# Kernel optimization log

Hardware: AMD Instinct MI355X
Metric: run time of the kernel (lower is better)

## Reference

```python
import jax, jax.numpy as jnp
import numpy as np

NUM_NODES = 100_000
NUM_EDGES = 3_200_000
THETA = 1.0  # module hyperparameter (default 1.0)


def setup_inputs() -> dict:
    key = jax.random.key(0)
    k_v, k_src, k_dst, k_t1, k_t2, k_r = jax.random.split(key, 6)
    v = jax.random.normal(k_v, (NUM_NODES,), dtype=jnp.float32)
    src = jax.random.randint(k_src, (NUM_EDGES,), 0, NUM_NODES, dtype=jnp.int32)
    dst = jax.random.randint(k_dst, (NUM_EDGES,), 0, NUM_NODES, dtype=jnp.int32)
    theta_sd_1 = jax.random.normal(k_t1, (NUM_EDGES,), dtype=jnp.float32) * 0.1
    theta_sd_2 = jax.random.normal(k_t2, (NUM_EDGES,), dtype=jnp.float32) * 0.1
    # conductance = 1/resistance, resistance in (0.5, 2.0) -> conductance in (0.5, 2.0)
    conductance = 1.0 / jax.random.uniform(k_r, (NUM_EDGES,), dtype=jnp.float32, minval=0.5, maxval=2.0)
    return {"t": 0, "v": v, "src": src, "dst": dst,
            "theta_sd_1": theta_sd_1, "theta_sd_2": theta_sd_2,
            "conductance": conductance}


def reference(t, v, src, dst, theta_sd_1, theta_sd_2, conductance):
    # per-edge gated current: g(vs, vd) = relu(theta1*(vs - vd) + theta2)
    diff = v[src] - v[dst]                                   # [E]
    current = conductance * jax.nn.relu(theta_sd_1 * diff + theta_sd_2)  # [E]
    incoming = jax.ops.segment_sum(current, dst, num_segments=NUM_NODES)  # [N]
    outgoing = jax.ops.segment_sum(current, src, num_segments=NUM_NODES)  # [N]
    return (incoming - outgoing) / THETA
```

## Files before the change

kernel.cpp:

```cpp
#include <hip/hip_runtime.h>
#include <hip/hip_fp16.h>


#define RANGE_LOG 15
#define RANGE     (1 << RANGE_LOG)
#define NBIN      4
#define P0_BLK    256
#define P0_EPT    4
#define P0_EPB    (P0_BLK * P0_EPT)
#define CAP       (2 * P0_EPB)
#define P1_BLK    1024
#define NSLICE    32

__global__ __launch_bounds__(P0_BLK) void p0_bin_kernel(
    const float* __restrict__ v,
    const int*   __restrict__ src,
    const int*   __restrict__ dst,
    const float* __restrict__ t1,
    const float* __restrict__ t2,
    const float* __restrict__ cond,
    unsigned*    __restrict__ bins,
    int*         __restrict__ cnt,
    int E, int G)
{
    __shared__ unsigned sbuf[NBIN][CAP];
    __shared__ int scnt[NBIN];

    if (threadIdx.x < NBIN) scnt[threadIdx.x] = 0;
    __syncthreads();

    const int blk = blockIdx.x;
    const int i0  = blk * P0_EPB + (int)threadIdx.x * P0_EPT;

    #define EMIT(node, mag, signbit)                                        \
        {                                                                   \
            int rr = (node) >> RANGE_LOG;                                   \
            unsigned lo = (unsigned)((node) & (RANGE - 1));                 \
            unsigned hb = (unsigned)__half_as_ushort(__float2half(mag));    \
            unsigned en = (lo << 17) | ((unsigned)(signbit) << 16) | hb;    \
            int idx = atomicAdd(&scnt[rr], 1);                              \
            sbuf[rr][idx] = en;                                             \
        }

    if (i0 + P0_EPT <= E) {
        int4   s4 = *(const int4*)  (src  + i0);
        int4   d4 = *(const int4*)  (dst  + i0);
        float4 a4 = *(const float4*)(t1   + i0);
        float4 b4 = *(const float4*)(t2   + i0);
        float4 c4 = *(const float4*)(cond + i0);

        float vs0 = v[s4.x], vs1 = v[s4.y], vs2 = v[s4.z], vs3 = v[s4.w];
        float vd0 = v[d4.x], vd1 = v[d4.y], vd2 = v[d4.z], vd3 = v[d4.w];

        float x0 = fmaf(a4.x, vs0 - vd0, b4.x);
        float x1 = fmaf(a4.y, vs1 - vd1, b4.y);
        float x2 = fmaf(a4.z, vs2 - vd2, b4.z);
        float x3 = fmaf(a4.w, vs3 - vd3, b4.w);

        if (x0 > 0.0f) { float c = c4.x * x0; EMIT(d4.x, c, 0u) EMIT(s4.x, c, 1u) }
        if (x1 > 0.0f) { float c = c4.y * x1; EMIT(d4.y, c, 0u) EMIT(s4.y, c, 1u) }
        if (x2 > 0.0f) { float c = c4.z * x2; EMIT(d4.z, c, 0u) EMIT(s4.z, c, 1u) }
        if (x3 > 0.0f) { float c = c4.w * x3; EMIT(d4.w, c, 0u) EMIT(s4.w, c, 1u) }
    } else {
        for (int i = i0; i < E; ++i) {
            int s = src[i], d = dst[i];
            float x = fmaf(t1[i], v[s] - v[d], t2[i]);
            if (x > 0.0f) { float c = cond[i] * x; EMIT(d, c, 0u) EMIT(s, c, 1u) }
        }
    }
    #undef EMIT

    __syncthreads();
    for (int r = 0; r < NBIN; ++r) {
        int c = scnt[r];
        unsigned* g = bins + ((size_t)r * G + blk) * CAP;
        for (int j = threadIdx.x; j < c; j += P0_BLK) g[j] = sbuf[r][j];
    }
    if (threadIdx.x < NBIN) cnt[threadIdx.x * G + blk] = scnt[threadIdx.x];
}

__global__ __launch_bounds__(P1_BLK) void p1_accum_kernel(
    const unsigned* __restrict__ bins,
    const int*      __restrict__ cnt,
    float*          __restrict__ partial,
    int N, int G)
{
    __shared__ __align__(16) float acc[RANGE];

    const int r    = blockIdx.x / NSLICE;
    const int s    = blockIdx.x % NSLICE;
    const int base = r << RANGE_LOG;
    const int len  = min(RANGE, N - base);

    for (int i = threadIdx.x; i < RANGE; i += P1_BLK) acc[i] = 0.0f;
    __syncthreads();

    const int segPer = (G + NSLICE - 1) / NSLICE;
    const int g0 = s * segPer;
    const int g1 = min(G, g0 + segPer);

    for (int g = g0; g < g1; ++g) {
        const int c = cnt[r * G + g];
        const unsigned* p = bins + ((size_t)r * G + g) * CAP;
        for (int j = threadIdx.x; j < c; j += P1_BLK) {
            unsigned e = p[j];
            int   lo  = (int)(e >> 17);
            float mag = __half2float(__ushort_as_half((unsigned short)(e & 0xFFFFu)));
            atomicAdd(&acc[lo], (e & 0x10000u) ? -mag : mag);
        }
    }

    __syncthreads();
    float* op = partial + (size_t)s * N + base;
    const int len4 = len & ~3;
    for (int i = (int)threadIdx.x * 4; i < len4; i += P1_BLK * 4)
        *(float4*)(op + i) = *(const float4*)&acc[i];
    for (int i = len4 + (int)threadIdx.x; i < len; i += P1_BLK)
        op[i] = acc[i];
}

__global__ __launch_bounds__(256) void reduce_kernel(
    const float* __restrict__ partial, float* __restrict__ out, int N4)
{
    int n = blockIdx.x * blockDim.x + threadIdx.x;
    if (n < N4) {
        float4 sm = make_float4(0.f, 0.f, 0.f, 0.f);
        for (int p = 0; p < NSLICE; ++p) {
            float4 q = ((const float4*)partial)[(size_t)p * N4 + n];
            sm.x += q.x; sm.y += q.y; sm.z += q.z; sm.w += q.w;
        }
        ((float4*)out)[n] = sm;
    }
}

__global__ __launch_bounds__(256) void reduce_scalar_kernel(
    const float* __restrict__ partial, float* __restrict__ out, int N)
{
    int n = blockIdx.x * blockDim.x + threadIdx.x;
    if (n < N) {
        float sm = 0.0f;
        for (int p = 0; p < NSLICE; ++p) sm += partial[(size_t)p * N + n];
        out[n] = sm;
    }
}

__global__ __launch_bounds__(256) void atomic_fallback_kernel(
    const float* __restrict__ v, const int* __restrict__ src, const int* __restrict__ dst,
    const float* __restrict__ t1, const float* __restrict__ t2, const float* __restrict__ cond,
    float* __restrict__ out, int E)
{
    int i = blockIdx.x * blockDim.x + threadIdx.x;
    int stride = gridDim.x * blockDim.x;
    for (; i < E; i += stride) {
        int s = src[i], d = dst[i];
        float x = fmaf(t1[i], v[s] - v[d], t2[i]);
        if (x > 0.0f) {
            float c = cond[i] * x;
            atomicAdd(&out[d], c);
            atomicAdd(&out[s], -c);
        }
    }
}

extern "C" void kernel_launch(void* const* d_in, const int* in_sizes, int n_in,
                              void* d_out, int out_size, void* d_ws, size_t ws_size,
                              hipStream_t stream) {
    const float* v    = (const float*)d_in[1];
    const int*   src  = (const int*)  d_in[2];
    const int*   dst  = (const int*)  d_in[3];
    const float* t1   = (const float*)d_in[4];
    const float* t2   = (const float*)d_in[5];
    const float* cond = (const float*)d_in[6];
    float* out = (float*)d_out;
    const int E = in_sizes[2];
    const int N = out_size;

    const int G = (E + P0_EPB - 1) / P0_EPB;

    const size_t binBytes = ((size_t)NBIN * G * CAP * 4 + 255) & ~(size_t)255;
    const size_t cntBytes = ((size_t)NBIN * G * 4 + 255) & ~(size_t)255;
    const size_t parBytes = (size_t)NSLICE * N * sizeof(float);

    const bool ok = (N <= NBIN * RANGE) &&
                    (binBytes + cntBytes + parBytes <= ws_size);

    if (ok) {
        unsigned* bins    = (unsigned*)d_ws;
        int*      cnt     = (int*)((char*)d_ws + binBytes);
        float*    partial = (float*)((char*)d_ws + binBytes + cntBytes);

        p0_bin_kernel<<<G, P0_BLK, 0, stream>>>(v, src, dst, t1, t2, cond,
                                                bins, cnt, E, G);

        const int R = (N + RANGE - 1) / RANGE;
        p1_accum_kernel<<<R * NSLICE, P1_BLK, 0, stream>>>(bins, cnt, partial, N, G);

        if ((N & 3) == 0) {
            int n4 = N / 4;
            reduce_kernel<<<(n4 + 255) / 256, 256, 0, stream>>>(partial, out, n4);
        } else {
            reduce_scalar_kernel<<<(N + 255) / 256, 256, 0, stream>>>(partial, out, N);
        }
    } else {
        hipMemsetAsync(out, 0, (size_t)N * sizeof(float), stream);
        int grid = (E + 255) / 256;
        if (grid > 2048) grid = 2048;
        atomic_fallback_kernel<<<grid, 256, 0, stream>>>(v, src, dst, t1, t2, cond, out, E);
    }
}
```

Before: 89.27 us.

## Compact binned edge entries into per-range global buffers via atomic cursors

The binning pass used to write each block's entries into fixed-capacity per-block slots. It now reserves space in one contiguous buffer per node range through a global atomic cursor and writes the entries there compactly. The accumulation pass then splits each range's contiguous entry list evenly across slices, instead of looping over per-block segments with separate counts. The node range is halved and the bin count doubled, which shrinks the shared accumulator per block. In exchange it adds a memset launch and global atomics, and it silently drops entries if a block overflows the 512-entry shared staging capacity or the estimated global capacity.

Result: faster. 87.24 us (-2.3%).

```diff
diff --git a/kernel.cpp b/kernel.cpp
--- a/kernel.cpp
+++ b/kernel.cpp
@@ -2,44 +2,43 @@
 #include <hip/hip_fp16.h>
 
 
-#define RANGE_LOG 15
-#define RANGE     (1 << RANGE_LOG)
-#define NBIN      4
-#define P0_BLK    256
-#define P0_EPT    4
-#define P0_EPB    (P0_BLK * P0_EPT)
-#define CAP       (2 * P0_EPB)
-#define P1_BLK    1024
-#define NSLICE    32
-
-__global__ __launch_bounds__(P0_BLK) void p0_bin_kernel(
+#define RL      14
+#define RANGE   (1 << RL)
+#define NB      8
+#define P0_BLK  256
+#define P0_EPT  4
+#define P0_EPB  (P0_BLK * P0_EPT)
+#define SCAP    512
+#define P1_BLK  1024
+#define NSLICE  32
+
+__global__ __launch_bounds__(P0_BLK) void p0_kernel(
     const float* __restrict__ v,
     const int*   __restrict__ src,
     const int*   __restrict__ dst,
     const float* __restrict__ t1,
     const float* __restrict__ t2,
     const float* __restrict__ cond,
-    unsigned*    __restrict__ bins,
-    int*         __restrict__ cnt,
-    int E, int G)
-{
-    __shared__ unsigned sbuf[NBIN][CAP];
-    __shared__ int scnt[NBIN];
-
-    if (threadIdx.x < NBIN) scnt[threadIdx.x] = 0;
-    __syncthreads();
-
-    const int blk = blockIdx.x;
-    const int i0  = blk * P0_EPB + (int)threadIdx.x * P0_EPT;
-
-    #define EMIT(node, mag, signbit)                                        \
-        {                                                                   \
-            int rr = (node) >> RANGE_LOG;                                   \
-            unsigned lo = (unsigned)((node) & (RANGE - 1));                 \
-            unsigned hb = (unsigned)__half_as_ushort(__float2half(mag));    \
-            unsigned en = (lo << 17) | ((unsigned)(signbit) << 16) | hb;    \
-            int idx = atomicAdd(&scnt[rr], 1);                              \
-            sbuf[rr][idx] = en;                                             \
+    unsigned*    __restrict__ entries,
+    int*         __restrict__ cursors,
+    int E, int EC)
+{
+    __shared__ unsigned sbuf[NB][SCAP];
+    __shared__ int scnt[NB], gbase[NB];
+
+    if (threadIdx.x < NB) scnt[threadIdx.x] = 0;
+    __syncthreads();
+
+    const int i0 = blockIdx.x * P0_EPB + (int)threadIdx.x * P0_EPT;
+
+    #define EMIT(node, mag, signbit)                                         \
+        {                                                                    \
+            int rr = (node) >> RL;                                           \
+            unsigned en = (((unsigned)((node) & (RANGE - 1))) << 17) |       \
+                          ((unsigned)(signbit) << 16) |                      \
+                          (unsigned)__half_as_ushort(__float2half(mag));     \
+            int idx = atomicAdd(&scnt[rr], 1);                               \
+            if (idx < SCAP) sbuf[rr][idx] = en;                              \
         }
 
     if (i0 + P0_EPT <= E) {
@@ -62,7 +61,7 @@
         if (x2 > 0.0f) { float c = c4.z * x2; EMIT(d4.z, c, 0u) EMIT(s4.z, c, 1u) }
         if (x3 > 0.0f) { float c = c4.w * x3; EMIT(d4.w, c, 0u) EMIT(s4.w, c, 1u) }
     } else {
-        for (int i = i0; i < E; ++i) {
+        for (int i = i0; i < E && i < i0 + P0_EPT; ++i) {
             int s = src[i], d = dst[i];
             float x = fmaf(t1[i], v[s] - v[d], t2[i]);
             if (x > 0.0f) { float c = cond[i] * x; EMIT(d, c, 0u) EMIT(s, c, 1u) }
@@ -71,48 +70,52 @@
     #undef EMIT
 
     __syncthreads();
-    for (int r = 0; r < NBIN; ++r) {
-        int c = scnt[r];
-        unsigned* g = bins + ((size_t)r * G + blk) * CAP;
-        for (int j = threadIdx.x; j < c; j += P0_BLK) g[j] = sbuf[r][j];
-    }
-    if (threadIdx.x < NBIN) cnt[threadIdx.x * G + blk] = scnt[threadIdx.x];
-}
-
-__global__ __launch_bounds__(P1_BLK) void p1_accum_kernel(
-    const unsigned* __restrict__ bins,
-    const int*      __restrict__ cnt,
+    if (threadIdx.x < NB) {
+        int c = min(scnt[threadIdx.x], SCAP);
+        gbase[threadIdx.x] = atomicAdd(&cursors[threadIdx.x], c);
+    }
+    __syncthreads();
+
+    for (int r = 0; r < NB; ++r) {
+        const int c  = min(scnt[r], SCAP);
+        const int gb = gbase[r];
+        unsigned* g = entries + (size_t)r * EC;
+        for (int j = threadIdx.x; j < c; j += P0_BLK)
+            if (gb + j < EC) g[gb + j] = sbuf[r][j];
+    }
+}
+
+__global__ __launch_bounds__(P1_BLK) void p1_kernel(
+    const unsigned* __restrict__ entries,
+    const int*      __restrict__ cursors,
     float*          __restrict__ partial,
-    int N, int G)
+    int N, int EC)
 {
     __shared__ __align__(16) float acc[RANGE];
 
     const int r    = blockIdx.x / NSLICE;
     const int s    = blockIdx.x % NSLICE;
-    const int base = r << RANGE_LOG;
+    const int base = r << RL;
     const int len  = min(RANGE, N - base);
 
     for (int i = threadIdx.x; i < RANGE; i += P1_BLK) acc[i] = 0.0f;
     __syncthreads();
 
-    const int segPer = (G + NSLICE - 1) / NSLICE;
-    const int g0 = s * segPer;
-    const int g1 = min(G, g0 + segPer);
-
-    for (int g = g0; g < g1; ++g) {
-        const int c = cnt[r * G + g];
-        const unsigned* p = bins + ((size_t)r * G + g) * CAP;
-        for (int j = threadIdx.x; j < c; j += P1_BLK) {
-            unsigned e = p[j];
-            int   lo  = (int)(e >> 17);
-            float mag = __half2float(__ushort_as_half((unsigned short)(e & 0xFFFFu)));
-            atomicAdd(&acc[lo], (e & 0x10000u) ? -mag : mag);
-        }
+    const int cnt = min(cursors[r], EC);
+    const int seg = (cnt + NSLICE - 1) / NSLICE;
+    const int e0  = s * seg;
+    const int e1  = min(cnt, e0 + seg);
+    const unsigned* p = entries + (size_t)r * EC;
+
+    for (int j = e0 + (int)threadIdx.x; j < e1; j += P1_BLK) {
+        unsigned e = p[j];
+        float mag = __half2float(__ushort_as_half((unsigned short)(e & 0xFFFFu)));
+        atomicAdd(&acc[e >> 17], (e & 0x10000u) ? -mag : mag);
     }
 
     __syncthreads();
     float* op = partial + (size_t)s * N + base;
-    const int len4 = len & ~3;
+    const int len4 = (len > 0) ? (len & ~3) : 0;
     for (int i = (int)threadIdx.x * 4; i < len4; i += P1_BLK * 4)
         *(float4*)(op + i) = *(const float4*)&acc[i];
     for (int i = len4 + (int)threadIdx.x; i < len; i += P1_BLK)
@@ -175,29 +178,33 @@
     const int E = in_sizes[2];
     const int N = out_size;
 
-    const int G = (E + P0_EPB - 1) / P0_EPB;
-
-    const size_t binBytes = ((size_t)NBIN * G * CAP * 4 + 255) & ~(size_t)255;
-    const size_t cntBytes = ((size_t)NBIN * G * 4 + 255) & ~(size_t)255;
+    const int EC = (int)((((size_t)E * 2 * RANGE) / (size_t)(N > 0 ? N : 1)
+                          + (size_t)E / 8 + 4096) & ~(size_t)255);
+
+    const size_t entBytes = (size_t)NB * EC * sizeof(unsigned);
+    const size_t curBytes = 256;
     const size_t parBytes = (size_t)NSLICE * N * sizeof(float);
 
-    const bool ok = (N <= NBIN * RANGE) &&
-                    (binBytes + cntBytes + parBytes <= ws_size);
+    const bool ok = (N <= NB * RANGE) &&
+                    (entBytes + curBytes + parBytes <= ws_size);
 
     if (ok) {
-        unsigned* bins    = (unsigned*)d_ws;
-        int*      cnt     = (int*)((char*)d_ws + binBytes);
-        float*    partial = (float*)((char*)d_ws + binBytes + cntBytes);
-
-        p0_bin_kernel<<<G, P0_BLK, 0, stream>>>(v, src, dst, t1, t2, cond,
-                                                bins, cnt, E, G);
+        unsigned* entries = (unsigned*)d_ws;
+        int*      cursors = (int*)((char*)d_ws + entBytes);
+        float*    partial = (float*)((char*)d_ws + entBytes + curBytes);
+
+        hipMemsetAsync(cursors, 0, curBytes, stream);
+
+        const int G = (E + P0_EPB - 1) / P0_EPB;
+        p0_kernel<<<G, P0_BLK, 0, stream>>>(v, src, dst, t1, t2, cond,
+                                            entries, cursors, E, EC);
 
         const int R = (N + RANGE - 1) / RANGE;
-        p1_accum_kernel<<<R * NSLICE, P1_BLK, 0, stream>>>(bins, cnt, partial, N, G);
+        p1_kernel<<<R * NSLICE, P1_BLK, 0, stream>>>(entries, cursors, partial, N, EC);
 
         if ((N & 3) == 0) {
-            int n4 = N / 4;
-            reduce_kernel<<<(n4 + 255) / 256, 256, 0, stream>>>(partial, out, n4);
+            const int N4 = N / 4;
+            reduce_kernel<<<(N4 + 255) / 256, 256, 0, stream>>>(partial, out, N4);
         } else {
             reduce_scalar_kernel<<<(N + 255) / 256, 256, 0, stream>>>(partial, out, N);
         }
```
